# Kernel optimization log

Hardware: AMD Instinct MI355X
Metric: run time of the kernel (lower is better)

Reference implementation:

```python
import jax, jax.numpy as jnp
import numpy as np

MAX_BOXES_PER_IMAGE = 200
NMS_IOU_THRESHOLD = 0.45
CONFIDENCE_THRESHOLD = 0.01
NEG = jnp.float32(-1e9)

B, N, C = 32, 24564, 81  # batch, anchors, classes (incl background)


def setup_inputs() -> dict:
    key = jax.random.key(0)
    k1, k2, k3 = jax.random.split(key, 3)
    logits = jax.random.normal(k1, (B, N, 4 + C), dtype=jnp.float32)
    # anchors in corner format [x0, y0, x1, y1], valid boxes in [0,1]
    centers = jax.random.uniform(k2, (N, 2), dtype=jnp.float32)
    sizes = jax.random.uniform(k3, (N, 2), dtype=jnp.float32) * 0.3 + 0.02
    anchors = jnp.clip(jnp.concatenate([centers - sizes / 2, centers + sizes / 2], axis=-1), 0.0, 1.0)
    return {"logits": logits, "anchors": anchors}


def decode_boxes(loc, anchors):
    # anchors [N,4] corners -> center/size; loc [B,N,4] offsets (no variance scaling, per source)
    cxcy = (anchors[:, 2:4] + anchors[:, 0:2]) / 2  # [N,2]
    wh = anchors[:, 2:4] - anchors[:, 0:2]          # [N,2]
    ctr = loc[..., 0:2] * wh + cxcy                 # [B,N,2]
    sz = jnp.exp(loc[..., 2:4]) * wh                # [B,N,2]
    boxes = jnp.concatenate([ctr - sz / 2, ctr + sz / 2], axis=-1)
    return jnp.clip(boxes, 0.0, 1.0)


def nms_single(boxes, scores):
    # boxes [N,4] corners, scores [N] (already -inf for background / below-threshold)
    area = (boxes[:, 2] - boxes[:, 0]) * (boxes[:, 3] - boxes[:, 1])

    def step(s, _):
        i = jnp.argmax(s)
        keep = s[i] > NEG / 2
        b = boxes[i]
        lt = jnp.maximum(b[:2], boxes[:, :2])
        rb = jnp.minimum(b[2:], boxes[:, 2:])
        whi = jnp.clip(rb - lt, 0.0)
        inter = whi[:, 0] * whi[:, 1]
        iou = inter / (area[i] + area - inter + 1e-9)
        s = jnp.where(iou > NMS_IOU_THRESHOLD, NEG, s).at[i].set(NEG)
        return s, (i, keep)

    _, (idx, keep) = jax.lax.scan(step, scores, None, length=MAX_BOXES_PER_IMAGE)
    return idx, keep  # [M], [M]


def reference(logits, anchors):
    loc = logits[..., :4]
    cls = jax.nn.softmax(logits[..., 4:], axis=-1)          # [B,N,C]
    scores = jnp.max(cls, axis=-1)                           # [B,N]
    classes = jnp.argmax(cls, axis=-1)                       # [B,N]
    boxes = decode_boxes(loc, anchors)                       # [B,N,4]
    # emulate boolean_mask(classes != 0) + score_threshold by masking scores
    valid = (classes != 0) & (scores >= CONFIDENCE_THRESHOLD)
    masked = jnp.where(valid, scores, NEG)
    idx, keep = jax.vmap(nms_single)(boxes, masked)          # [B,M]
    det_boxes = jax.vmap(lambda b, i: b[i])(boxes, idx) * keep[..., None].astype(boxes.dtype)
    det_scores = jax.vmap(lambda s, i: s[i])(scores, idx) * keep.astype(scores.dtype)
    det_classes = jax.vmap(lambda c, i: c[i])(classes, idx) * keep.astype(classes.dtype)
    det_num = jnp.sum(keep, axis=-1).astype(jnp.int32)
    return det_boxes, det_classes, det_scores, det_num
```

## Files before the change

### kernel.cpp

```cpp
#include <hip/hip_runtime.h>

#define Bn 32
#define Nn 24564
#define MAXB 200
#define NBIN 2048
#define CH 2048
#define NCHK 4
#define CHK_PRE 2
#define CHTOT (NCHK * CH)
#define CHPRE (CHK_PRE * CH)
#define INVK 0xFFFFFFFFu

typedef unsigned long long u64;
typedef unsigned int u32;

__device__ inline double fast_exp_d(double x) {
  const double LOG2E = 1.4426950408889634074;
  const double LN2   = 0.69314718055994530942;
  double t = x * LOG2E;
  double fi = floor(t + 0.5);
  double f = (t - fi) * LN2;
  double p = 2.505210838544172e-8;
  p = p * f + 2.755731922398589e-7;
  p = p * f + 2.7557319223985893e-6;
  p = p * f + 2.48015873015873e-5;
  p = p * f + 1.984126984126984e-4;
  p = p * f + 1.3888888888888889e-3;
  p = p * f + 8.333333333333333e-3;
  p = p * f + 4.1666666666666664e-2;
  p = p * f + 1.6666666666666666e-1;
  p = p * f + 0.5;
  p = p * f + 1.0;
  p = p * f + 1.0;
  long long e = (long long)fi;
  return p * __longlong_as_double((e + 1023LL) << 52);
}

__device__ inline double clip01(double v) {
  return v < 0.0 ? 0.0 : (v > 1.0 ? 1.0 : v);
}

__global__ __launch_bounds__(256) void w1_score(const float* __restrict__ logits,
                                                u32* __restrict__ keyA) {
  __shared__ float lds[64 * 85];
  const int tid = threadIdx.x;
  const int bx = blockIdx.x;
  const int b = bx / 384;
  const int n0 = (bx % 384) << 6;
  int cnt = Nn - n0;
  cnt = cnt > 64 ? 64 : cnt;
  const int nf4 = (cnt * 85) >> 2;
  const float4* src = reinterpret_cast<const float4*>(logits + ((size_t)b * Nn + n0) * 85);
  float4* dst = reinterpret_cast<float4*>(lds);
  for (int i = tid; i < nf4; i += 256) dst[i] = src[i];
  __syncthreads();

  const int g = tid >> 2;
  const int s = tid & 3;
  if (g < cnt) {
    const float* row = lds + g * 85;
    float mx = -1e30f; int ai = 1000;
    for (int c = s; c < 81; c += 4) {
      float v = row[4 + c];
      if (v > mx) { mx = v; ai = c; }
    }
    #pragma unroll
    for (int d = 1; d <= 2; d <<= 1) {
      float om = __shfl_xor(mx, d);
      int oi = __shfl_xor(ai, d);
      if (om > mx || (om == mx && oi < ai)) { mx = om; ai = oi; }
    }
    float sum = 0.f;
    for (int c = s; c < 81; c += 4) sum += __expf(row[4 + c] - mx);
    sum += __shfl_xor(sum, 1);
    sum += __shfl_xor(sum, 2);
    if (s == 0) {
      float sc = 1.0f / sum;
      u32 kv = INVK;
      if (ai != 0 && sc >= 0.00985f) kv = ~__float_as_uint(sc);
      keyA[(size_t)b * Nn + n0 + g] = kv;
    }
  }
}

__global__ __launch_bounds__(1024) void w3_cutcompact(const u32* __restrict__ keyA,
                                                      int* __restrict__ chunkCntG,
                                                      int* __restrict__ clist) {
  __shared__ int hist[NBIN];
  __shared__ int chunkIdL[NBIN];
  __shared__ int wsum[16];
  __shared__ int sBinHi;
  __shared__ int sCnt[NCHK];
  const int b = blockIdx.x;
  const int tid = threadIdx.x;
  const int lane = tid & 63, wid = tid >> 6;
  const u32* kb = keyA + (size_t)b * Nn;

  for (int i = tid; i < NBIN; i += 1024) hist[i] = 0;
  chunkIdL[2 * tid] = 255;
  chunkIdL[2 * tid + 1] = 255;
  if (tid < NCHK) sCnt[tid] = 0;
  __syncthreads();
  for (int i = tid; i < Nn; i += 1024) {
    u32 kv = kb[i];
    u32 bin = (kv - 0xC0000000u) >> 15;
    if (bin < NBIN) atomicAdd(&hist[bin], 1);
  }
  __syncthreads();

  int h0 = hist[2 * tid], h1 = hist[2 * tid + 1];
  int v = h0 + h1;
  int iv = v;
  #pragma unroll
  for (int d = 1; d < 64; d <<= 1) {
    int t = __shfl_up(iv, d);
    if (lane >= d) iv += t;
  }
  if (lane == 63) wsum[wid] = iv;
  __syncthreads();
  if (tid < 16) {
    int w = wsum[tid];
    #pragma unroll
    for (int d = 1; d < 16; d <<= 1) {
      int t = __shfl_up(w, d);
      if ((int)tid >= d) w += t;
    }
    wsum[tid] = w;
  }
  __syncthreads();
  int excl = iv - v + (wid > 0 ? wsum[wid - 1] : 0);
  hist[2 * tid] = excl + h0;
  hist[2 * tid + 1] = excl + h0 + h1;
  __syncthreads();

  int binLo = -1, cumBase = 0;
  for (int c = 0; c < NCHK; ++c) {
    if (tid == 0) sBinHi = binLo;
    __syncthreads();
    const int limit = cumBase + CH;
    int loc = -1;
    if (hist[2 * tid] <= limit) loc = 2 * tid;
    if (hist[2 * tid + 1] <= limit) loc = 2 * tid + 1;
    if (loc > binLo) atomicMax(&sBinHi, loc);
    __syncthreads();
    int binHi = sBinHi;
    if (binHi == binLo) binHi = binLo + 1;
    if (2 * tid > binLo && 2 * tid <= binHi) chunkIdL[2 * tid] = c;
    if (2 * tid + 1 > binLo && 2 * tid + 1 <= binHi) chunkIdL[2 * tid + 1] = c;
    cumBase = hist[(binHi < NBIN ? binHi : NBIN - 1)];
    binLo = binHi;
    __syncthreads();
  }

  for (int i0 = 0; i0 < Nn; i0 += 1024) {
    int i = i0 + tid;
    int c = 255;
    if (i < Nn) {
      u32 kv = kb[i];
      u32 bin = (kv - 0xC0000000u) >> 15;
      if (bin < NBIN) c = chunkIdL[bin];
    }
    #pragma unroll
    for (int cc = 0; cc < NCHK; ++cc) {
      bool pred = (c == cc);
      u64 m = __ballot(pred);
      if (m) {
        int base = 0;
        if (lane == 0) base = atomicAdd(&sCnt[cc], (int)__popcll(m));
        base = __shfl(base, 0);
        if (pred) {
          int off = (int)__popcll(m & ((1ULL << lane) - 1ULL));
          int p = base + off;
          if (p < CH) clist[b * CHTOT + cc * CH + p] = i;
        }
      }
    }
  }
  __syncthreads();
  if (tid < NCHK) chunkCntG[b * NCHK + tid] = sCnt[tid];
}

__global__ __launch_bounds__(256) void w4_rescore(const float* __restrict__ logits,
                                                  const float* __restrict__ anchors,
                                                  const int* __restrict__ clist,
                                                  const int* __restrict__ chunkCntG,
                                                  double* __restrict__ boxesd,
                                                  int* __restrict__ clsd,
                                                  u64* __restrict__ ekeysG) {
  const int tid = threadIdx.x;
  const int bx = blockIdx.x;
  const int b = bx >> 6;
  const int blk = bx & 63;
  const int c = blk >> 5;
  const int sb = (blk & 31) << 6;
  int cnt = chunkCntG[b * NCHK + c];
  cnt = cnt > CH ? CH : cnt;
  const int g = tid >> 2, s = tid & 3;
  const int slot = sb + g;
  u64 K = ~0ULL;
  if (slot < cnt) {
    const int n = clist[b * CHTOT + c * CH + slot];
    const float* row = logits + ((size_t)b * Nn + n) * 85;
    float rv[21];
    float mx = -1e30f; int ai = 1000;
    #pragma unroll
    for (int q = 0; q < 21; ++q) {
      int cc = s + 4 * q;
      float vv = (cc < 81) ? row[4 + cc] : -1e30f;
      rv[q] = vv;
      if (cc < 81 && vv > mx) { mx = vv; ai = cc; }
    }
    #pragma unroll
    for (int d = 1; d <= 2; d <<= 1) {
      float om = __shfl_xor(mx, d);
      int oi = __shfl_xor(ai, d);
      if (om > mx || (om == mx && oi < ai)) { mx = om; ai = oi; }
    }
    double sum = 0.0;
    #pragma unroll
    for (int q = 0; q < 21; ++q) {
      if (s + 4 * q < 81) sum += fast_exp_d((double)rv[q] - (double)mx);
    }
    sum += __shfl_xor(sum, 1);
    sum += __shfl_xor(sum, 2);
    if (s == 0) {
      double score = 1.0 / sum;
      if (ai != 0 && score >= 0.01) {
        float4 a4 = reinterpret_cast<const float4*>(anchors)[n];
        double ax1 = a4.x, ay1 = a4.y, ax2 = a4.z, ay2 = a4.w;
        double cx = (ax2 + ax1) * 0.5, cy = (ay2 + ay1) * 0.5;
        double ww = ax2 - ax1, hh = ay2 - ay1;
        double ctrx = (double)row[0] * ww + cx;
        double ctry = (double)row[1] * hh + cy;
        double szx = fast_exp_d((double)row[2]) * ww;
        double szy = fast_exp_d((double)row[3]) * hh;
        double* bp = boxesd + (size_t)(b * Nn + n) * 4;
        bp[0] = clip01(ctrx - szx * 0.5);
        bp[1] = clip01(ctry - szy * 0.5);
        bp[2] = clip01(ctrx + szx * 0.5);
        bp[3] = clip01(ctry + szy * 0.5);
        clsd[b * Nn + n] = ai;
        u64 sb2 = (u64)__double_as_longlong(score);
        u64 e4 = (sb2 >> 52) - 1015ULL;
        u64 mant45 = (sb2 & ((1ULL << 52) - 1)) >> 7;
        u64 flip = (~((e4 << 45) | mant45)) & ((1ULL << 49) - 1);
        K = (flip << 15) | (u64)n;
      }
    }
  }
  if (s == 0) ekeysG[(size_t)b * CHPRE + c * CH + slot] = K;
}

__global__ __launch_bounds__(1024) void w5_sortnms(const float* __restrict__ logits,
                                                   const float* __restrict__ anchors,
                                                   const u64* __restrict__ ekeysG,
                                                   const int* __restrict__ chunkCntG,
                                                   const int* __restrict__ clist,
                                                   double* __restrict__ boxesd,
                                                   int* __restrict__ clsd,
                                                   float* __restrict__ out) {
  __shared__ u64 ek[CH];
  __shared__ double bbuf[2][64][4];
  __shared__ u64 awv[16];
  __shared__ u64 killm[64];
  __shared__ double selBox[MAXB][4];
  __shared__ double selArea[MAXB];
  __shared__ float selScore[MAXB];
  __shared__ int selIdx[MAXB];
  __shared__ int sS;
  const int b = blockIdx.x;
  const int tid = threadIdx.x;
  const int lane = tid & 63, wid = tid >> 6;
  const double THR = 0.45;
  if (tid == 0) sS = 0;
  __syncthreads();

  for (int c = 0; c < NCHK; ++c) {
    if (sS >= MAXB) break;
    int cnt = chunkCntG[b * NCHK + c];
    cnt = cnt > CH ? CH : cnt;
    if (cnt == 0) break;

    if (c < CHK_PRE) {
      for (int i = tid; i < CH; i += 1024) ek[i] = ekeysG[(size_t)b * CHPRE + c * CH + i];
      __syncthreads();
    } else {
      for (int i = tid; i < CH; i += 1024) ek[i] = ~0ULL;
      __syncthreads();
      const int g = tid >> 2, s4 = tid & 3;
      #pragma unroll 1
      for (int pass = 0; pass < CH / 256; ++pass) {
        int slot = pass * 256 + g;
        if (slot < cnt) {
          const int n = clist[b * CHTOT + c * CH + slot];
          const float* row = logits + ((size_t)b * Nn + n) * 85;
          float rv[21];
          float mx = -1e30f; int ai = 1000;
          #pragma unroll
          for (int q = 0; q < 21; ++q) {
            int cc = s4 + 4 * q;
            float vv = (cc < 81) ? row[4 + cc] : -1e30f;
            rv[q] = vv;
            if (cc < 81 && vv > mx) { mx = vv; ai = cc; }
          }
          #pragma unroll
          for (int d = 1; d <= 2; d <<= 1) {
            float om = __shfl_xor(mx, d);
            int oi = __shfl_xor(ai, d);
            if (om > mx || (om == mx && oi < ai)) { mx = om; ai = oi; }
          }
          double sum = 0.0;
          #pragma unroll
          for (int q = 0; q < 21; ++q) {
            if (s4 + 4 * q < 81) sum += fast_exp_d((double)rv[q] - (double)mx);
          }
          sum += __shfl_xor(sum, 1);
          sum += __shfl_xor(sum, 2);
          if (s4 == 0) {
            u64 K = ~0ULL;
            double score = 1.0 / sum;
            if (ai != 0 && score >= 0.01) {
              float4 a4 = reinterpret_cast<const float4*>(anchors)[n];
              double ax1 = a4.x, ay1 = a4.y, ax2 = a4.z, ay2 = a4.w;
              double cx = (ax2 + ax1) * 0.5, cy = (ay2 + ay1) * 0.5;
              double ww = ax2 - ax1, hh = ay2 - ay1;
              double ctrx = (double)row[0] * ww + cx;
              double ctry = (double)row[1] * hh + cy;
              double szx = fast_exp_d((double)row[2]) * ww;
              double szy = fast_exp_d((double)row[3]) * hh;
              double* bp = boxesd + (size_t)(b * Nn + n) * 4;
              bp[0] = clip01(ctrx - szx * 0.5);
              bp[1] = clip01(ctry - szy * 0.5);
              bp[2] = clip01(ctrx + szx * 0.5);
              bp[3] = clip01(ctry + szy * 0.5);
              clsd[b * Nn + n] = ai;
              u64 sb2 = (u64)__double_as_longlong(score);
              u64 e4 = (sb2 >> 52) - 1015ULL;
              u64 mant45 = (sb2 & ((1ULL << 52) - 1)) >> 7;
              u64 flip = (~((e4 << 45) | mant45)) & ((1ULL << 49) - 1);
              K = (flip << 15) | (u64)n;
            }
            ek[slot] = K;
          }
        }
      }
      __syncthreads();
    }

    int P2 = 64;
    while (P2 < cnt) P2 <<= 1;
    for (int k = 2; k <= P2; k <<= 1) {
      for (int j = k >> 1; j >= 1; j >>= 1) {
        if (tid < (P2 >> 1)) {
          int l = ((tid & ~(j - 1)) << 1) | (tid & (j - 1));
          int r = l | j;
          bool up = ((l & k) == 0);
          u64 a = ek[l], bbv = ek[r];
          if ((a > bbv) == up) { ek[l] = bbv; ek[r] = a; }
        }
        __syncthreads();
      }
    }

    int pos = 0, bf = 0;
    if (tid < 256) {
      int ci = tid >> 2, comp = tid & 3;
      u64 Kc = ek[ci];
      double vv = 0.0;
      if (Kc != ~0ULL) vv = boxesd[(size_t)(b * Nn + (int)(Kc & 0x7FFF)) * 4 + comp];
      bbuf[0][ci][comp] = vv;
    }
    __syncthreads();
    for (;;) {
      int S = sS;
      if (S >= MAXB || pos >= CH) break;
      u64 K = ek[pos + lane];
      bool valid = (K != ~0ULL);
      if (!__any(valid)) break;

      if (tid < 256 && pos + 64 < CH) {
        int ci = tid >> 2, comp = tid & 3;
        u64 Kc = ek[pos + 64 + ci];
        double vv = 0.0;
        if (Kc != ~0ULL) vv = boxesd[(size_t)(b * Nn + (int)(Kc & 0x7FFF)) * 4 + comp];
        bbuf[bf ^ 1][ci][comp] = vv;
      }

      double cx1 = bbuf[bf][lane][0], cy1 = bbuf[bf][lane][1];
      double cx2 = bbuf[bf][lane][2], cy2 = bbuf[bf][lane][3];
      double carea = (cx2 - cx1) * (cy2 - cy1);

      bool aliveL = true;
      for (int k = wid; k < S; k += 16) {
        double ltx = fmax(selBox[k][0], cx1), lty = fmax(selBox[k][1], cy1);
        double rbx = fmin(selBox[k][2], cx2), rby = fmin(selBox[k][3], cy2);
        double w = rbx - ltx; w = w < 0 ? 0 : w;
        double h = rby - lty; h = h < 0 ? 0 : h;
        double inter = w * h;
        double denom = selArea[k] + carea - inter + 1e-9;
        if (inter > THR * denom) aliveL = false;
      }
      u64 aw = __ballot(aliveL);
      if (lane == 0) awv[wid] = aw;

      #pragma unroll
      for (int q = 0; q < 4; ++q) {
        int j = (wid << 2) | q;
        double jx1 = bbuf[bf][j][0], jy1 = bbuf[bf][j][1];
        double jx2 = bbuf[bf][j][2], jy2 = bbuf[bf][j][3];
        double jar = (jx2 - jx1) * (jy2 - jy1);
        double ltx = fmax(jx1, cx1), lty = fmax(jy1, cy1);
        double rbx = fmin(jx2, cx2), rby = fmin(jy2, cy2);
        double w = rbx - ltx; w = w < 0 ? 0 : w;
        double h = rby - lty; h = h < 0 ? 0 : h;
        double inter = w * h;
        double denom = jar + carea - inter + 1e-9;
        u64 km = __ballot(inter > THR * denom);
        if (lane == 0) killm[j] = km;
      }
      __syncthreads();

      if (tid < 64) {
        u64 alive = __ballot(valid);
        #pragma unroll
        for (int w = 0; w < 16; ++w) alive &= awv[w];
        u64 m = alive;
        int Sl = S;
        while (m != 0 && Sl < MAXB) {
          int j = __ffsll((unsigned long long)m) - 1;
          if (lane == 0) {
            double jx1 = bbuf[bf][j][0], jy1 = bbuf[bf][j][1];
            double jx2 = bbuf[bf][j][2], jy2 = bbuf[bf][j][3];
            u64 Kj = ek[pos + j];
            u64 key49 = (~(Kj >> 15)) & ((1ULL << 49) - 1);
            u64 e = (key49 >> 45) + 1015ULL;
            u64 mant = (key49 & ((1ULL << 45) - 1)) << 7;
            selBox[Sl][0] = jx1; selBox[Sl][1] = jy1;
            selBox[Sl][2] = jx2; selBox[Sl][3] = jy2;
            selArea[Sl] = (jx2 - jx1) * (jy2 - jy1);
            selScore[Sl] = (float)__longlong_as_double((long long)((e << 52) | mant));
            selIdx[Sl] = (int)(Kj & 0x7FFF);
          }
          Sl++;
          m &= ~(1ULL << j);
          m &= ~killm[j];
        }
        if (lane == 0) sS = Sl;
      }
      __syncthreads();
      bf ^= 1;
      pos += 64;
    }
    __syncthreads();
  }

  const int S = sS;
  float* det_boxes = out;
  float* det_classes = out + Bn * MAXB * 4;
  float* det_scores = out + Bn * MAXB * 4 + Bn * MAXB;
  float* det_num = out + Bn * MAXB * 4 + 2 * Bn * MAXB;
  for (int k = tid; k < MAXB; k += 1024) {
    int o = b * MAXB + k;
    if (k < S) {
      det_boxes[o * 4 + 0] = (float)selBox[k][0];
      det_boxes[o * 4 + 1] = (float)selBox[k][1];
      det_boxes[o * 4 + 2] = (float)selBox[k][2];
      det_boxes[o * 4 + 3] = (float)selBox[k][3];
      det_classes[o] = (float)clsd[b * Nn + selIdx[k]];
      det_scores[o] = selScore[k];
    } else {
      det_boxes[o * 4 + 0] = 0.f; det_boxes[o * 4 + 1] = 0.f;
      det_boxes[o * 4 + 2] = 0.f; det_boxes[o * 4 + 3] = 0.f;
      det_classes[o] = 0.f;
      det_scores[o] = 0.f;
    }
  }
  if (tid == 0) det_num[b] = (float)S;
}

extern "C" void kernel_launch(void* const* d_in, const int* in_sizes, int n_in,
                              void* d_out, int out_size, void* d_ws, size_t ws_size,
                              hipStream_t stream) {
  const float* logits = (const float*)d_in[0];
  const float* anchors = (const float*)d_in[1];
  float* out = (float*)d_out;
  char* ws = (char*)d_ws;

  double* boxesd = (double*)ws;
  size_t off = (size_t)Bn * Nn * 4 * sizeof(double);
  int* clsd    = (int*)(ws + off);  off += (size_t)Bn * Nn * sizeof(int);
  u32* keyA    = (u32*)(ws + off);  off += (size_t)Bn * Nn * sizeof(u32);
  int* chunkCnt= (int*)(ws + off);  off += (size_t)Bn * NCHK * sizeof(int);
  int* clist   = (int*)(ws + off);  off += (size_t)Bn * CHTOT * sizeof(int);
  u64* ekeysG  = (u64*)(ws + off);

  w1_score     <<<dim3(Bn * 384), dim3(256),  0, stream>>>(logits, keyA);
  w3_cutcompact<<<dim3(Bn),       dim3(1024), 0, stream>>>(keyA, chunkCnt, clist);
  w4_rescore   <<<dim3(Bn * 64),  dim3(256),  0, stream>>>(logits, anchors, clist, chunkCnt,
                                                           boxesd, clsd, ekeysG);
  w5_sortnms   <<<dim3(Bn),       dim3(1024), 0, stream>>>(logits, anchors, ekeysG, chunkCnt,
                                                           clist, boxesd, clsd, out);
}
```

Measured before the change: 174.7 us.

## Presort 256-key segments in rescore kernel and merge them in sortnms

The rescore kernel now launches a quarter as many blocks, and each block processes 256 slots over four passes. Each block bitonic-sorts its 256 keys in shared memory before writing them out. The per-image sort kernel then only runs the merge stages (256→2048) for the precomputed chunks instead of a full bitonic sort. This moves sort work from the 32-block serial kernel into the widely parallel rescore kernel, at the cost of fewer rescore blocks and extra syncs there.

```diff
diff --git a/kernel.cpp b/kernel.cpp
--- a/kernel.cpp
+++ b/kernel.cpp
@@ -40,7 +40,7 @@
   return v < 0.0 ? 0.0 : (v > 1.0 ? 1.0 : v);
 }
 
-__global__ __launch_bounds__(256) void w1_score(const float* __restrict__ logits,
+__global__ __launch_bounds__(256) void x1_score(const float* __restrict__ logits,
                                                 u32* __restrict__ keyA) {
   __shared__ float lds[64 * 85];
   const int tid = threadIdx.x;
@@ -83,7 +83,7 @@
   }
 }
 
-__global__ __launch_bounds__(1024) void w3_cutcompact(const u32* __restrict__ keyA,
+__global__ __launch_bounds__(1024) void x3_cutcompact(const u32* __restrict__ keyA,
                                                       int* __restrict__ chunkCntG,
                                                       int* __restrict__ clist) {
   __shared__ int hist[NBIN];
@@ -180,78 +180,99 @@
   if (tid < NCHK) chunkCntG[b * NCHK + tid] = sCnt[tid];
 }
 
-__global__ __launch_bounds__(256) void w4_rescore(const float* __restrict__ logits,
+__global__ __launch_bounds__(256) void x4_rescore(const float* __restrict__ logits,
                                                   const float* __restrict__ anchors,
                                                   const int* __restrict__ clist,
                                                   const int* __restrict__ chunkCntG,
                                                   double* __restrict__ boxesd,
                                                   int* __restrict__ clsd,
                                                   u64* __restrict__ ekeysG) {
+  __shared__ u64 ekseg[256];
   const int tid = threadIdx.x;
   const int bx = blockIdx.x;
-  const int b = bx >> 6;
-  const int blk = bx & 63;
-  const int c = blk >> 5;
-  const int sb = (blk & 31) << 6;
+  const int b = bx >> 4;
+  const int blk = bx & 15;
+  const int c = blk >> 3;
+  const int seg = blk & 7;
   int cnt = chunkCntG[b * NCHK + c];
   cnt = cnt > CH ? CH : cnt;
   const int g = tid >> 2, s = tid & 3;
-  const int slot = sb + g;
-  u64 K = ~0ULL;
-  if (slot < cnt) {
-    const int n = clist[b * CHTOT + c * CH + slot];
-    const float* row = logits + ((size_t)b * Nn + n) * 85;
-    float rv[21];
-    float mx = -1e30f; int ai = 1000;
-    #pragma unroll
-    for (int q = 0; q < 21; ++q) {
-      int cc = s + 4 * q;
-      float vv = (cc < 81) ? row[4 + cc] : -1e30f;
-      rv[q] = vv;
-      if (cc < 81 && vv > mx) { mx = vv; ai = cc; }
-    }
-    #pragma unroll
-    for (int d = 1; d <= 2; d <<= 1) {
-      float om = __shfl_xor(mx, d);
-      int oi = __shfl_xor(ai, d);
-      if (om > mx || (om == mx && oi < ai)) { mx = om; ai = oi; }
-    }
-    double sum = 0.0;
-    #pragma unroll
-    for (int q = 0; q < 21; ++q) {
-      if (s + 4 * q < 81) sum += fast_exp_d((double)rv[q] - (double)mx);
-    }
-    sum += __shfl_xor(sum, 1);
-    sum += __shfl_xor(sum, 2);
-    if (s == 0) {
-      double score = 1.0 / sum;
-      if (ai != 0 && score >= 0.01) {
-        float4 a4 = reinterpret_cast<const float4*>(anchors)[n];
-        double ax1 = a4.x, ay1 = a4.y, ax2 = a4.z, ay2 = a4.w;
-        double cx = (ax2 + ax1) * 0.5, cy = (ay2 + ay1) * 0.5;
-        double ww = ax2 - ax1, hh = ay2 - ay1;
-        double ctrx = (double)row[0] * ww + cx;
-        double ctry = (double)row[1] * hh + cy;
-        double szx = fast_exp_d((double)row[2]) * ww;
-        double szy = fast_exp_d((double)row[3]) * hh;
-        double* bp = boxesd + (size_t)(b * Nn + n) * 4;
-        bp[0] = clip01(ctrx - szx * 0.5);
-        bp[1] = clip01(ctry - szy * 0.5);
-        bp[2] = clip01(ctrx + szx * 0.5);
-        bp[3] = clip01(ctry + szy * 0.5);
-        clsd[b * Nn + n] = ai;
-        u64 sb2 = (u64)__double_as_longlong(score);
-        u64 e4 = (sb2 >> 52) - 1015ULL;
-        u64 mant45 = (sb2 & ((1ULL << 52) - 1)) >> 7;
-        u64 flip = (~((e4 << 45) | mant45)) & ((1ULL << 49) - 1);
-        K = (flip << 15) | (u64)n;
-      }
-    }
-  }
-  if (s == 0) ekeysG[(size_t)b * CHPRE + c * CH + slot] = K;
-}
-
-__global__ __launch_bounds__(1024) void w5_sortnms(const float* __restrict__ logits,
+
+  #pragma unroll 1
+  for (int pass = 0; pass < 4; ++pass) {
+    const int slot = seg * 256 + pass * 64 + g;
+    u64 K = ~0ULL;
+    if (slot < cnt) {
+      const int n = clist[b * CHTOT + c * CH + slot];
+      const float* row = logits + ((size_t)b * Nn + n) * 85;
+      float rv[21];
+      float mx = -1e30f; int ai = 1000;
+      #pragma unroll
+      for (int q = 0; q < 21; ++q) {
+        int cc = s + 4 * q;
+        float vv = (cc < 81) ? row[4 + cc] : -1e30f;
+        rv[q] = vv;
+        if (cc < 81 && vv > mx) { mx = vv; ai = cc; }
+      }
+      #pragma unroll
+      for (int d = 1; d <= 2; d <<= 1) {
+        float om = __shfl_xor(mx, d);
+        int oi = __shfl_xor(ai, d);
+        if (om > mx || (om == mx && oi < ai)) { mx = om; ai = oi; }
+      }
+      double sum = 0.0;
+      #pragma unroll
+      for (int q = 0; q < 21; ++q) {
+        if (s + 4 * q < 81) sum += fast_exp_d((double)rv[q] - (double)mx);
+      }
+      sum += __shfl_xor(sum, 1);
+      sum += __shfl_xor(sum, 2);
+      if (s == 0) {
+        double score = 1.0 / sum;
+        if (ai != 0 && score >= 0.01) {
+          float4 a4 = reinterpret_cast<const float4*>(anchors)[n];
+          double ax1 = a4.x, ay1 = a4.y, ax2 = a4.z, ay2 = a4.w;
+          double cx = (ax2 + ax1) * 0.5, cy = (ay2 + ay1) * 0.5;
+          double ww = ax2 - ax1, hh = ay2 - ay1;
+          double ctrx = (double)row[0] * ww + cx;
+          double ctry = (double)row[1] * hh + cy;
+          double szx = fast_exp_d((double)row[2]) * ww;
+          double szy = fast_exp_d((double)row[3]) * hh;
+          double* bp = boxesd + (size_t)(b * Nn + n) * 4;
+          bp[0] = clip01(ctrx - szx * 0.5);
+          bp[1] = clip01(ctry - szy * 0.5);
+          bp[2] = clip01(ctrx + szx * 0.5);
+          bp[3] = clip01(ctry + szy * 0.5);
+          clsd[b * Nn + n] = ai;
+          u64 sb2 = (u64)__double_as_longlong(score);
+          u64 e4 = (sb2 >> 52) - 1015ULL;
+          u64 mant45 = (sb2 & ((1ULL << 52) - 1)) >> 7;
+          u64 flip = (~((e4 << 45) | mant45)) & ((1ULL << 49) - 1);
+          K = (flip << 15) | (u64)n;
+        }
+      }
+    }
+    if (s == 0) ekseg[pass * 64 + g] = K;
+  }
+  __syncthreads();
+
+  for (int k = 2; k <= 256; k <<= 1) {
+    for (int j = k >> 1; j >= 1; j >>= 1) {
+      if (tid < 128) {
+        int l = ((tid & ~(j - 1)) << 1) | (tid & (j - 1));
+        int r = l | j;
+        bool up = ((l & k) == 0);
+        u64 a = ekseg[l], bv = ekseg[r];
+        if ((a > bv) == up) { ekseg[l] = bv; ekseg[r] = a; }
+      }
+      __syncthreads();
+    }
+  }
+  u64* dstp = ekeysG + (size_t)b * CHPRE + c * CH + seg * 256;
+  for (int i = tid; i < 256; i += 256) dstp[i] = ekseg[i];
+}
+
+__global__ __launch_bounds__(1024) void x5_sortnms(const float* __restrict__ logits,
                                                    const float* __restrict__ anchors,
                                                    const u64* __restrict__ ekeysG,
                                                    const int* __restrict__ chunkCntG,
@@ -284,6 +305,21 @@
     if (c < CHK_PRE) {
       for (int i = tid; i < CH; i += 1024) ek[i] = ekeysG[(size_t)b * CHPRE + c * CH + i];
       __syncthreads();
+      for (int L = 256; L <= 1024; L <<= 1) {
+        int pair = tid / L, i = tid % L;
+        int base = pair * 2 * L;
+        int l = base + i, r = base + 2 * L - 1 - i;
+        u64 a = ek[l], bv = ek[r];
+        if (a > bv) { ek[l] = bv; ek[r] = a; }
+        __syncthreads();
+        for (int j = L >> 1; j >= 1; j >>= 1) {
+          int ll = ((tid & ~(j - 1)) << 1) | (tid & (j - 1));
+          int rr = ll | j;
+          u64 x = ek[ll], y = ek[rr];
+          if (x > y) { ek[ll] = y; ek[rr] = x; }
+          __syncthreads();
+        }
+      }
     } else {
       for (int i = tid; i < CH; i += 1024) ek[i] = ~0ULL;
       __syncthreads();
@@ -345,20 +381,19 @@
         }
       }
       __syncthreads();
-    }
-
-    int P2 = 64;
-    while (P2 < cnt) P2 <<= 1;
-    for (int k = 2; k <= P2; k <<= 1) {
-      for (int j = k >> 1; j >= 1; j >>= 1) {
-        if (tid < (P2 >> 1)) {
-          int l = ((tid & ~(j - 1)) << 1) | (tid & (j - 1));
-          int r = l | j;
-          bool up = ((l & k) == 0);
-          u64 a = ek[l], bbv = ek[r];
-          if ((a > bbv) == up) { ek[l] = bbv; ek[r] = a; }
+      int P2 = 64;
+      while (P2 < cnt) P2 <<= 1;
+      for (int k = 2; k <= P2; k <<= 1) {
+        for (int j = k >> 1; j >= 1; j >>= 1) {
+          if (tid < (P2 >> 1)) {
+            int l = ((tid & ~(j - 1)) << 1) | (tid & (j - 1));
+            int r = l | j;
+            bool up = ((l & k) == 0);
+            u64 a = ek[l], bbv = ek[r];
+            if ((a > bbv) == up) { ek[l] = bbv; ek[r] = a; }
+          }
+          __syncthreads();
         }
-        __syncthreads();
       }
     }
 
@@ -494,10 +529,10 @@
   int* clist   = (int*)(ws + off);  off += (size_t)Bn * CHTOT * sizeof(int);
   u64* ekeysG  = (u64*)(ws + off);
 
-  w1_score     <<<dim3(Bn * 384), dim3(256),  0, stream>>>(logits, keyA);
-  w3_cutcompact<<<dim3(Bn),       dim3(1024), 0, stream>>>(keyA, chunkCnt, clist);
-  w4_rescore   <<<dim3(Bn * 64),  dim3(256),  0, stream>>>(logits, anchors, clist, chunkCnt,
+  x1_score     <<<dim3(Bn * 384), dim3(256),  0, stream>>>(logits, keyA);
+  x3_cutcompact<<<dim3(Bn),       dim3(1024), 0, stream>>>(keyA, chunkCnt, clist);
+  x4_rescore   <<<dim3(Bn * 16),  dim3(256),  0, stream>>>(logits, anchors, clist, chunkCnt,
                                                            boxesd, clsd, ekeysG);
-  w5_sortnms   <<<dim3(Bn),       dim3(1024), 0, stream>>>(logits, anchors, ekeysG, chunkCnt,
+  x5_sortnms   <<<dim3(Bn),       dim3(1024), 0, stream>>>(logits, anchors, ekeysG, chunkCnt,
                                                            clist, boxesd, clsd, out);
 }
```

After: 171.2 us. -2.0%, faster.
